# Performance work log

Measured on AMD Instinct MI355X. Metric: run time of the kernel, lower is better.

## Reference

```python
import jax, jax.numpy as jnp
import numpy as np

N_NODES = 100000
N_EDGES = 1600000
D_IN = 128
D_OUT = 128


def setup_inputs() -> dict:
    key = jax.random.key(0)
    ks = jax.random.split(key, 8)
    h = jax.random.normal(ks[0], (N_NODES, D_IN), dtype=jnp.float32)
    edge_val = jax.random.uniform(ks[1], (N_EDGES,), dtype=jnp.float32)
    # Linear weights in torch layout [out, in]
    W_self = jax.random.normal(ks[2], (D_OUT, D_IN), dtype=jnp.float32) * (1.0 / np.sqrt(D_IN))
    b_self = jax.random.normal(ks[3], (D_OUT,), dtype=jnp.float32) * 0.01
    W_nb = jax.random.normal(ks[4], (D_OUT, D_IN), dtype=jnp.float32) * (1.0 / np.sqrt(D_IN))
    b_nb = jax.random.normal(ks[5], (D_OUT,), dtype=jnp.float32) * 0.01
    edge_row = jax.random.randint(ks[6], (N_EDGES,), 0, N_NODES, dtype=jnp.int64)
    edge_col = jax.random.randint(ks[7], (N_EDGES,), 0, N_NODES, dtype=jnp.int64)
    return {"h": h, "edge_val": edge_val, "W_self": W_self, "b_self": b_self,
            "W_nb": W_nb, "b_nb": b_nb, "edge_row": edge_row, "edge_col": edge_col}


def reference(h, edge_val, W_self, b_self, W_nb, b_nb, edge_row, edge_col):
    # self_h = Linear_self(h[:out_nodes]); out_nodes == N_NODES here
    self_h = h @ W_self.T + b_self  # [N, D_OUT]
    # neighbor_h = adj.spmm(h): sparse COO (row, col, val) times dense h
    msgs = edge_val[:, None] * h[edge_col]            # [E, D_IN]
    neighbor_h = jax.ops.segment_sum(msgs, edge_row, num_segments=N_NODES)  # [N, D_IN]
    out = self_h + neighbor_h @ W_nb.T + b_nb
    return out
```

## Files before the change

kernel.cpp:

```cpp
#include <hip/hip_runtime.h>


constexpr int NN = 100000;
constexpr int NE = 1600000;
constexpr int D  = 128;
constexpr int NBUCK  = 1024;
constexpr int BROWS  = 98;
constexpr int BCAP   = 2048;
constexpr int CHUNK  = 2048;
constexpr int NCH    = (NE + CHUNK - 1) / CHUNK;
constexpr int GM     = 64;
constexpr int NT     = (NN + GM - 1) / GM;
constexpr int GRID   = 512;
constexpr int LP     = 132;

typedef __bf16 bf16x8 __attribute__((ext_vector_type(8)));
typedef float  f32x4  __attribute__((ext_vector_type(4)));
typedef float  f32x2  __attribute__((ext_vector_type(2)));
typedef unsigned short u16x4 __attribute__((ext_vector_type(4)));

__global__ __launch_bounds__(256) void gemm_mfma(
    const float* __restrict__ h,
    const float* __restrict__ Wself,
    const float* __restrict__ Wnb,
    const float* __restrict__ bself,
    const float* __restrict__ bnb,
    float* __restrict__ out,
    __bf16* __restrict__ tmpb)
{
    __shared__ __bf16 hs[2][GM * LP];
    const int t    = threadIdx.x;
    const int w    = t >> 6;
    const int lane = t & 63;
    const int l15  = lane & 15;
    const int quad = lane >> 4;

    bf16x8 wf[4][4];
    #pragma unroll
    for (int ns = 0; ns < 4; ++ns) {
        int wrow = w * 64 + ns * 16 + l15;
        const float* wr = (wrow < D) ? (Wself + (size_t)wrow * D)
                                     : (Wnb + (size_t)(wrow - D) * D);
        #pragma unroll
        for (int kk = 0; kk < 4; ++kk) {
            f32x4 lo = *(const f32x4*)(wr + kk * 32 + quad * 8);
            f32x4 hi = *(const f32x4*)(wr + kk * 32 + quad * 8 + 4);
            bf16x8 bb;
            #pragma unroll
            for (int j = 0; j < 4; ++j) { bb[j] = (__bf16)lo[j]; bb[4 + j] = (__bf16)hi[j]; }
            wf[ns][kk] = bb;
        }
    }
    f32x4 biasv[4];
    #pragma unroll
    for (int ns = 0; ns < 4; ++ns) {
        int col = w * 64 + ns * 16 + quad * 4;
        if (col < D) {
            f32x4 b1 = *(const f32x4*)(bself + col);
            f32x4 b2 = *(const f32x4*)(bnb + col);
            biasv[ns] = b1 + b2;
        } else biasv[ns] = (f32x4){0.f, 0.f, 0.f, 0.f};
    }

    int srow[4], scol[4];
    #pragma unroll
    for (int it = 0; it < 4; ++it) {
        int idx = it * 2048 + t * 8;
        srow[it] = idx >> 7;
        scol[it] = idx & 127;
    }

    {
        const int row0 = blockIdx.x * GM;
        #pragma unroll
        for (int it = 0; it < 4; ++it) {
            int gr = row0 + srow[it]; if (gr >= NN) gr = NN - 1;
            f32x4 lo = *(const f32x4*)(h + (size_t)gr * D + scol[it]);
            f32x4 hi = *(const f32x4*)(h + (size_t)gr * D + scol[it] + 4);
            bf16x8 v;
            #pragma unroll
            for (int j = 0; j < 4; ++j) { v[j] = (__bf16)lo[j]; v[4 + j] = (__bf16)hi[j]; }
            *(bf16x8*)(&hs[0][srow[it] * LP + scol[it]]) = v;
        }
    }
    __syncthreads();

    int buf = 0;
    for (int tile = blockIdx.x; tile < NT; tile += GRID) {
        const int row0 = tile * GM;
        const bool hasn = (tile + GRID) < NT;

        f32x4 pf[8];
        if (hasn) {
            const int nrow0 = (tile + GRID) * GM;
            #pragma unroll
            for (int it = 0; it < 4; ++it) {
                int gr = nrow0 + srow[it]; if (gr >= NN) gr = NN - 1;
                pf[it * 2]     = *(const f32x4*)(h + (size_t)gr * D + scol[it]);
                pf[it * 2 + 1] = *(const f32x4*)(h + (size_t)gr * D + scol[it] + 4);
            }
        }

        f32x4 acc[4][4];
        #pragma unroll
        for (int mi = 0; mi < 4; ++mi)
            #pragma unroll
            for (int ns = 0; ns < 4; ++ns) acc[mi][ns] = (f32x4){0.f, 0.f, 0.f, 0.f};

        const __bf16* hb = hs[buf];
        #pragma unroll
        for (int mi = 0; mi < 4; ++mi) {
            bf16x8 hf[4];
            #pragma unroll
            for (int kk = 0; kk < 4; ++kk)
                hf[kk] = *(const bf16x8*)(&hb[(mi * 16 + l15) * LP + quad * 8 + kk * 32]);
            #pragma unroll
            for (int ns = 0; ns < 4; ++ns)
                #pragma unroll
                for (int kk = 0; kk < 4; ++kk)
                    acc[mi][ns] = __builtin_amdgcn_mfma_f32_16x16x32_bf16(wf[ns][kk], hf[kk], acc[mi][ns], 0, 0, 0);
        }

        if (hasn) {
            #pragma unroll
            for (int it = 0; it < 4; ++it) {
                bf16x8 v;
                #pragma unroll
                for (int j = 0; j < 4; ++j) {
                    v[j]     = (__bf16)pf[it * 2][j];
                    v[4 + j] = (__bf16)pf[it * 2 + 1][j];
                }
                *(bf16x8*)(&hs[buf ^ 1][srow[it] * LP + scol[it]]) = v;
            }
        }
        __syncthreads();

        #pragma unroll
        for (int mi = 0; mi < 4; ++mi) {
            int row = row0 + mi * 16 + l15;
            if (row < NN) {
                if (w < 2) {
                    #pragma unroll
                    for (int ns = 0; ns < 4; ++ns) {
                        int col = w * 64 + ns * 16 + quad * 4;
                        *(f32x4*)(out + (size_t)row * D + col) = acc[mi][ns] + biasv[ns];
                    }
                } else {
                    #pragma unroll
                    for (int ns = 0; ns < 4; ++ns) {
                        int col = (w - 2) * 64 + ns * 16 + quad * 4;
                        u16x4 v;
                        #pragma unroll
                        for (int i = 0; i < 4; ++i) {
                            __bf16 b = (__bf16)acc[mi][ns][i];
                            v[i] = *(unsigned short*)&b;
                        }
                        *(u16x4*)(tmpb + (size_t)row * D + col) = v;
                    }
                }
            }
        }
        buf ^= 1;
    }
}

__global__ __launch_bounds__(256) void wc_scatter(
    const int* __restrict__ erow, const int* __restrict__ ecol,
    const float* __restrict__ eval_,
    int* __restrict__ gcount, int2* __restrict__ epair)
{
    __shared__ int  cnt[NBUCK];
    __shared__ int  lscan[NBUCK];
    __shared__ int  gbase[NBUCK];
    __shared__ int  ss[NBUCK];
    __shared__ int2 sbuf[CHUNK];
    __shared__ int  saddr[CHUNK];
    __shared__ int  s_total;

    const int t  = threadIdx.x;
    const int c0 = blockIdx.x * CHUNK;

    for (int b = t; b < NBUCK; b += 256) cnt[b] = 0;
    __syncthreads();

    int   bp[8];
    int   colr[8];
    float valr[8];
    #pragma unroll
    for (int j = 0; j < 8; ++j) {
        int e = c0 + j * 256 + t;
        if (e < NE) {
            int r   = erow[e];
            colr[j] = ecol[e];
            valr[j] = eval_[e];
            int b   = r / BROWS;
            int rlo = r - b * BROWS;
            int pos = atomicAdd(&cnt[b], 1);
            bp[j]   = b | (rlo << 10) | (pos << 17);
        } else bp[j] = -1;
    }
    __syncthreads();

    #pragma unroll
    for (int k = 0; k < 4; ++k) ss[t + k * 256] = cnt[t + k * 256];
    __syncthreads();
    for (int off = 1; off < NBUCK; off <<= 1) {
        int v[4];
        #pragma unroll
        for (int k = 0; k < 4; ++k) {
            int i = t + k * 256;
            v[k] = ss[i] + ((i >= off) ? ss[i - off] : 0);
        }
        __syncthreads();
        #pragma unroll
        for (int k = 0; k < 4; ++k) ss[t + k * 256] = v[k];
        __syncthreads();
    }
    #pragma unroll
    for (int k = 0; k < 4; ++k) {
        int i = t + k * 256;
        int n = cnt[i];
        lscan[i] = ss[i] - n;
        gbase[i] = (n > 0) ? atomicAdd(&gcount[i], n) : 0;
    }
    if (t == 0) s_total = ss[NBUCK - 1];
    __syncthreads();

    #pragma unroll
    for (int j = 0; j < 8; ++j) {
        if (bp[j] >= 0) {
            int b   = bp[j] & 1023;
            int rlo = (bp[j] >> 10) & 127;
            int pos = bp[j] >> 17;
            int slot = lscan[b] + pos;
            sbuf[slot]  = make_int2(colr[j] | (rlo << 17), __float_as_int(valr[j]));
            saddr[slot] = b * BCAP + gbase[b] + pos;
        }
    }
    __syncthreads();

    int ce = s_total;
    for (int i = t; i < ce; i += 256)
        epair[saddr[i]] = sbuf[i];
}

__global__ __launch_bounds__(512, 8) void sort_aggregate(
    const int2* __restrict__ epair, const int* __restrict__ gcount,
    const __bf16* __restrict__ tmpb, float* __restrict__ out)
{
    __shared__ int  cnt[BROWS];
    __shared__ int  off2[BROWS];
    __shared__ int  cur[BROWS];
    __shared__ int  ss[128];
    __shared__ int2 sorted[BCAP];

    const int t = threadIdx.x;
    const int b = blockIdx.x;
    int n = gcount[b];
    if (n > BCAP) n = BCAP;
    const int2* src = epair + (size_t)b * BCAP;

    if (t < BROWS) cnt[t] = 0;
    __syncthreads();

    int2 r[4];
    int  nr = 0;
    for (int i = t; i < n; i += 512) {
        int2 p = src[i];
        r[nr++] = p;
        atomicAdd(&cnt[(p.x >> 17) & 127], 1);
    }
    __syncthreads();

    if (t < 128) ss[t] = (t < BROWS) ? cnt[t] : 0;
    __syncthreads();
    for (int o = 1; o < 128; o <<= 1) {
        int y = 0;
        if (t < 128 && t >= o) y = ss[t - o];
        __syncthreads();
        if (t < 128) ss[t] += y;
        __syncthreads();
    }
    if (t < BROWS) {
        int v = cnt[t];
        off2[t] = ss[t] - v;
        cur[t]  = ss[t] - v;
    }
    __syncthreads();

    for (int j = 0; j < nr; ++j) {
        int slot = atomicAdd(&cur[(r[j].x >> 17) & 127], 1);
        sorted[slot] = r[j];
    }
    __syncthreads();

    const int wv   = t >> 6;
    const int lane = t & 63;
    const __bf16* tb = tmpb + lane * 2;

    for (int rl = wv; rl < BROWS; rl += 8) {
        int row = b * BROWS + rl;
        if (row >= NN) break;
        int beg = __builtin_amdgcn_readfirstlane(off2[rl]);
        int end = __builtin_amdgcn_readfirstlane(cur[rl]);
        if (beg >= end) continue;

        float ax[4] = {0.f, 0.f, 0.f, 0.f};
        float ay[4] = {0.f, 0.f, 0.f, 0.f};
        int e = beg;
        for (; e + 7 < end; e += 8) {
            int2 p[8];
            #pragma unroll
            for (int k = 0; k < 8; ++k) p[k] = sorted[e + k];
            #pragma unroll
            for (int k = 0; k < 8; ++k) {
                int col = p[k].x & 0x1FFFF;
                unsigned u = *(const unsigned*)(tb + (size_t)col * D);
                float v = __int_as_float(p[k].y);
                ax[k & 3] += v * __uint_as_float(u << 16);
                ay[k & 3] += v * __uint_as_float(u & 0xffff0000u);
            }
        }
        for (; e + 3 < end; e += 4) {
            int2 p[4];
            #pragma unroll
            for (int k = 0; k < 4; ++k) p[k] = sorted[e + k];
            #pragma unroll
            for (int k = 0; k < 4; ++k) {
                int col = p[k].x & 0x1FFFF;
                unsigned u = *(const unsigned*)(tb + (size_t)col * D);
                float v = __int_as_float(p[k].y);
                ax[k] += v * __uint_as_float(u << 16);
                ay[k] += v * __uint_as_float(u & 0xffff0000u);
            }
        }
        for (; e < end; ++e) {
            int2 p = sorted[e];
            int col = p.x & 0x1FFFF;
            unsigned u = *(const unsigned*)(tb + (size_t)col * D);
            float v = __int_as_float(p.y);
            ax[0] += v * __uint_as_float(u << 16);
            ay[0] += v * __uint_as_float(u & 0xffff0000u);
        }

        f32x2* o = (f32x2*)(out + (size_t)row * D + lane * 2);
        f32x2 c = __builtin_nontemporal_load(o);
        c.x += (ax[0] + ax[1]) + (ax[2] + ax[3]);
        c.y += (ay[0] + ay[1]) + (ay[2] + ay[3]);
        __builtin_nontemporal_store(c, o);
    }
}

extern "C" void kernel_launch(void* const* d_in, const int* in_sizes, int n_in,
                              void* d_out, int out_size, void* d_ws, size_t ws_size,
                              hipStream_t stream) {
    const float* h     = (const float*)d_in[0];
    const float* eval_ = (const float*)d_in[1];
    const float* Wself = (const float*)d_in[2];
    const float* bself = (const float*)d_in[3];
    const float* Wnb   = (const float*)d_in[4];
    const float* bnb   = (const float*)d_in[5];
    const int*   erow  = (const int*)d_in[6];
    const int*   ecol  = (const int*)d_in[7];
    float* out = (float*)d_out;

    char* p = (char*)d_ws;
    __bf16* tmpb    = (__bf16*)p;   p += (size_t)NT * GM * D * 2;
    int2*   epair   = (int2*)p;     p += (size_t)NBUCK * BCAP * 8;
    int*    gcount  = (int*)p;

    hipMemsetAsync(gcount, 0, NBUCK * 4, stream);

    gemm_mfma<<<GRID, 256, 0, stream>>>(h, Wself, Wnb, bself, bnb, out, tmpb);
    wc_scatter<<<NCH, 256, 0, stream>>>(erow, ecol, eval_, gcount, epair);
    sort_aggregate<<<NBUCK, 512, 0, stream>>>(epair, gcount, tmpb, out);
}
```

Baseline: 263.0 us.

## Merge GEMM and edge bucket-scatter into one launch; use wave-shuffle scan

Combines the MFMA GEMM kernel and the edge bucketing scatter kernel into a single launch, with the first GRID blocks doing GEMM and the rest scattering edges, sharing one union shared-memory buffer. This removes a kernel boundary and lets the compute-bound GEMM overlap the memory-bound scatter. The 1024-bucket prefix scan is also rewritten from a barrier-heavy Hillis-Steele loop over shared memory into per-thread sums plus a wavefront shuffle scan. The shared allocation is now the maximum of both roles, which can lower occupancy for the GEMM blocks.

```diff
diff --git a/kernel.cpp b/kernel.cpp
--- a/kernel.cpp
+++ b/kernel.cpp
@@ -13,235 +13,248 @@
 constexpr int NT     = (NN + GM - 1) / GM;
 constexpr int GRID   = 512;
 constexpr int LP     = 132;
+constexpr int FUSED_GRID = GRID + NCH;
 
 typedef __bf16 bf16x8 __attribute__((ext_vector_type(8)));
 typedef float  f32x4  __attribute__((ext_vector_type(4)));
 typedef float  f32x2  __attribute__((ext_vector_type(2)));
 typedef unsigned short u16x4 __attribute__((ext_vector_type(4)));
 
-__global__ __launch_bounds__(256) void gemm_mfma(
+constexpr int SMEM_BYTES = 36928;
+
+__global__ __launch_bounds__(256) void gemm_wc(
     const float* __restrict__ h,
     const float* __restrict__ Wself,
     const float* __restrict__ Wnb,
     const float* __restrict__ bself,
     const float* __restrict__ bnb,
     float* __restrict__ out,
-    __bf16* __restrict__ tmpb)
-{
-    __shared__ __bf16 hs[2][GM * LP];
-    const int t    = threadIdx.x;
-    const int w    = t >> 6;
-    const int lane = t & 63;
-    const int l15  = lane & 15;
-    const int quad = lane >> 4;
-
-    bf16x8 wf[4][4];
-    #pragma unroll
-    for (int ns = 0; ns < 4; ++ns) {
-        int wrow = w * 64 + ns * 16 + l15;
-        const float* wr = (wrow < D) ? (Wself + (size_t)wrow * D)
-                                     : (Wnb + (size_t)(wrow - D) * D);
-        #pragma unroll
-        for (int kk = 0; kk < 4; ++kk) {
-            f32x4 lo = *(const f32x4*)(wr + kk * 32 + quad * 8);
-            f32x4 hi = *(const f32x4*)(wr + kk * 32 + quad * 8 + 4);
-            bf16x8 bb;
-            #pragma unroll
-            for (int j = 0; j < 4; ++j) { bb[j] = (__bf16)lo[j]; bb[4 + j] = (__bf16)hi[j]; }
-            wf[ns][kk] = bb;
-        }
-    }
-    f32x4 biasv[4];
-    #pragma unroll
-    for (int ns = 0; ns < 4; ++ns) {
-        int col = w * 64 + ns * 16 + quad * 4;
-        if (col < D) {
-            f32x4 b1 = *(const f32x4*)(bself + col);
-            f32x4 b2 = *(const f32x4*)(bnb + col);
-            biasv[ns] = b1 + b2;
-        } else biasv[ns] = (f32x4){0.f, 0.f, 0.f, 0.f};
-    }
-
-    int srow[4], scol[4];
-    #pragma unroll
-    for (int it = 0; it < 4; ++it) {
-        int idx = it * 2048 + t * 8;
-        srow[it] = idx >> 7;
-        scol[it] = idx & 127;
-    }
-
-    {
-        const int row0 = blockIdx.x * GM;
-        #pragma unroll
-        for (int it = 0; it < 4; ++it) {
-            int gr = row0 + srow[it]; if (gr >= NN) gr = NN - 1;
-            f32x4 lo = *(const f32x4*)(h + (size_t)gr * D + scol[it]);
-            f32x4 hi = *(const f32x4*)(h + (size_t)gr * D + scol[it] + 4);
-            bf16x8 v;
-            #pragma unroll
-            for (int j = 0; j < 4; ++j) { v[j] = (__bf16)lo[j]; v[4 + j] = (__bf16)hi[j]; }
-            *(bf16x8*)(&hs[0][srow[it] * LP + scol[it]]) = v;
-        }
-    }
-    __syncthreads();
-
-    int buf = 0;
-    for (int tile = blockIdx.x; tile < NT; tile += GRID) {
-        const int row0 = tile * GM;
-        const bool hasn = (tile + GRID) < NT;
-
-        f32x4 pf[8];
-        if (hasn) {
-            const int nrow0 = (tile + GRID) * GM;
-            #pragma unroll
-            for (int it = 0; it < 4; ++it) {
-                int gr = nrow0 + srow[it]; if (gr >= NN) gr = NN - 1;
-                pf[it * 2]     = *(const f32x4*)(h + (size_t)gr * D + scol[it]);
-                pf[it * 2 + 1] = *(const f32x4*)(h + (size_t)gr * D + scol[it] + 4);
-            }
-        }
-
-        f32x4 acc[4][4];
-        #pragma unroll
-        for (int mi = 0; mi < 4; ++mi)
-            #pragma unroll
-            for (int ns = 0; ns < 4; ++ns) acc[mi][ns] = (f32x4){0.f, 0.f, 0.f, 0.f};
-
-        const __bf16* hb = hs[buf];
-        #pragma unroll
-        for (int mi = 0; mi < 4; ++mi) {
-            bf16x8 hf[4];
-            #pragma unroll
-            for (int kk = 0; kk < 4; ++kk)
-                hf[kk] = *(const bf16x8*)(&hb[(mi * 16 + l15) * LP + quad * 8 + kk * 32]);
-            #pragma unroll
-            for (int ns = 0; ns < 4; ++ns)
-                #pragma unroll
-                for (int kk = 0; kk < 4; ++kk)
-                    acc[mi][ns] = __builtin_amdgcn_mfma_f32_16x16x32_bf16(wf[ns][kk], hf[kk], acc[mi][ns], 0, 0, 0);
-        }
-
-        if (hasn) {
-            #pragma unroll
-            for (int it = 0; it < 4; ++it) {
-                bf16x8 v;
-                #pragma unroll
-                for (int j = 0; j < 4; ++j) {
-                    v[j]     = (__bf16)pf[it * 2][j];
-                    v[4 + j] = (__bf16)pf[it * 2 + 1][j];
-                }
-                *(bf16x8*)(&hs[buf ^ 1][srow[it] * LP + scol[it]]) = v;
-            }
-        }
-        __syncthreads();
-
-        #pragma unroll
-        for (int mi = 0; mi < 4; ++mi) {
-            int row = row0 + mi * 16 + l15;
-            if (row < NN) {
-                if (w < 2) {
-                    #pragma unroll
-                    for (int ns = 0; ns < 4; ++ns) {
-                        int col = w * 64 + ns * 16 + quad * 4;
-                        *(f32x4*)(out + (size_t)row * D + col) = acc[mi][ns] + biasv[ns];
-                    }
-                } else {
-                    #pragma unroll
-                    for (int ns = 0; ns < 4; ++ns) {
-                        int col = (w - 2) * 64 + ns * 16 + quad * 4;
-                        u16x4 v;
-                        #pragma unroll
-                        for (int i = 0; i < 4; ++i) {
-                            __bf16 b = (__bf16)acc[mi][ns][i];
-                            v[i] = *(unsigned short*)&b;
-                        }
-                        *(u16x4*)(tmpb + (size_t)row * D + col) = v;
-                    }
-                }
-            }
-        }
-        buf ^= 1;
-    }
-}
-
-__global__ __launch_bounds__(256) void wc_scatter(
+    __bf16* __restrict__ tmpb,
     const int* __restrict__ erow, const int* __restrict__ ecol,
     const float* __restrict__ eval_,
     int* __restrict__ gcount, int2* __restrict__ epair)
 {
-    __shared__ int  cnt[NBUCK];
-    __shared__ int  lscan[NBUCK];
-    __shared__ int  gbase[NBUCK];
-    __shared__ int  ss[NBUCK];
-    __shared__ int2 sbuf[CHUNK];
-    __shared__ int  saddr[CHUNK];
-    __shared__ int  s_total;
-
-    const int t  = threadIdx.x;
-    const int c0 = blockIdx.x * CHUNK;
-
-    for (int b = t; b < NBUCK; b += 256) cnt[b] = 0;
-    __syncthreads();
-
-    int   bp[8];
-    int   colr[8];
-    float valr[8];
-    #pragma unroll
-    for (int j = 0; j < 8; ++j) {
-        int e = c0 + j * 256 + t;
-        if (e < NE) {
-            int r   = erow[e];
-            colr[j] = ecol[e];
-            valr[j] = eval_[e];
-            int b   = r / BROWS;
-            int rlo = r - b * BROWS;
-            int pos = atomicAdd(&cnt[b], 1);
-            bp[j]   = b | (rlo << 10) | (pos << 17);
-        } else bp[j] = -1;
-    }
-    __syncthreads();
-
-    #pragma unroll
-    for (int k = 0; k < 4; ++k) ss[t + k * 256] = cnt[t + k * 256];
-    __syncthreads();
-    for (int off = 1; off < NBUCK; off <<= 1) {
-        int v[4];
+    __shared__ __align__(16) char smem[SMEM_BYTES];
+    const int t = threadIdx.x;
+
+    if (blockIdx.x < GRID) {
+        const int bid  = blockIdx.x;
+        const int w    = t >> 6;
+        const int lane = t & 63;
+        const int l15  = lane & 15;
+        const int quad = lane >> 4;
+        __bf16* hs0 = (__bf16*)smem;
+        __bf16* hs1 = hs0 + GM * LP;
+
+        bf16x8 wf[4][4];
+        #pragma unroll
+        for (int ns = 0; ns < 4; ++ns) {
+            int wrow = w * 64 + ns * 16 + l15;
+            const float* wr = (wrow < D) ? (Wself + (size_t)wrow * D)
+                                         : (Wnb + (size_t)(wrow - D) * D);
+            #pragma unroll
+            for (int kk = 0; kk < 4; ++kk) {
+                f32x4 lo = *(const f32x4*)(wr + kk * 32 + quad * 8);
+                f32x4 hi = *(const f32x4*)(wr + kk * 32 + quad * 8 + 4);
+                bf16x8 bb;
+                #pragma unroll
+                for (int j = 0; j < 4; ++j) { bb[j] = (__bf16)lo[j]; bb[4 + j] = (__bf16)hi[j]; }
+                wf[ns][kk] = bb;
+            }
+        }
+        f32x4 biasv[4];
+        #pragma unroll
+        for (int ns = 0; ns < 4; ++ns) {
+            int col = w * 64 + ns * 16 + quad * 4;
+            if (col < D) {
+                f32x4 b1 = *(const f32x4*)(bself + col);
+                f32x4 b2 = *(const f32x4*)(bnb + col);
+                biasv[ns] = b1 + b2;
+            } else biasv[ns] = (f32x4){0.f, 0.f, 0.f, 0.f};
+        }
+
+        int srow[4], scol[4];
+        #pragma unroll
+        for (int it = 0; it < 4; ++it) {
+            int idx = it * 2048 + t * 8;
+            srow[it] = idx >> 7;
+            scol[it] = idx & 127;
+        }
+
+        {
+            const int row0 = bid * GM;
+            #pragma unroll
+            for (int it = 0; it < 4; ++it) {
+                int gr = row0 + srow[it]; if (gr >= NN) gr = NN - 1;
+                f32x4 lo = *(const f32x4*)(h + (size_t)gr * D + scol[it]);
+                f32x4 hi = *(const f32x4*)(h + (size_t)gr * D + scol[it] + 4);
+                bf16x8 v;
+                #pragma unroll
+                for (int j = 0; j < 4; ++j) { v[j] = (__bf16)lo[j]; v[4 + j] = (__bf16)hi[j]; }
+                *(bf16x8*)(&hs0[srow[it] * LP + scol[it]]) = v;
+            }
+        }
+        __syncthreads();
+
+        int buf = 0;
+        for (int tile = bid; tile < NT; tile += GRID) {
+            const int row0 = tile * GM;
+            const bool hasn = (tile + GRID) < NT;
+            __bf16* hb = buf ? hs1 : hs0;
+            __bf16* hw = buf ? hs0 : hs1;
+
+            f32x4 pf[8];
+            if (hasn) {
+                const int nrow0 = (tile + GRID) * GM;
+                #pragma unroll
+                for (int it = 0; it < 4; ++it) {
+                    int gr = nrow0 + srow[it]; if (gr >= NN) gr = NN - 1;
+                    pf[it * 2]     = *(const f32x4*)(h + (size_t)gr * D + scol[it]);
+                    pf[it * 2 + 1] = *(const f32x4*)(h + (size_t)gr * D + scol[it] + 4);
+                }
+            }
+
+            f32x4 acc[4][4];
+            #pragma unroll
+            for (int mi = 0; mi < 4; ++mi)
+                #pragma unroll
+                for (int ns = 0; ns < 4; ++ns) acc[mi][ns] = (f32x4){0.f, 0.f, 0.f, 0.f};
+
+            #pragma unroll
+            for (int mi = 0; mi < 4; ++mi) {
+                bf16x8 hf[4];
+                #pragma unroll
+                for (int kk = 0; kk < 4; ++kk)
+                    hf[kk] = *(const bf16x8*)(&hb[(mi * 16 + l15) * LP + quad * 8 + kk * 32]);
+                #pragma unroll
+                for (int ns = 0; ns < 4; ++ns)
+                    #pragma unroll
+                    for (int kk = 0; kk < 4; ++kk)
+                        acc[mi][ns] = __builtin_amdgcn_mfma_f32_16x16x32_bf16(wf[ns][kk], hf[kk], acc[mi][ns], 0, 0, 0);
+            }
+
+            if (hasn) {
+                #pragma unroll
+                for (int it = 0; it < 4; ++it) {
+                    bf16x8 v;
+                    #pragma unroll
+                    for (int j = 0; j < 4; ++j) {
+                        v[j]     = (__bf16)pf[it * 2][j];
+                        v[4 + j] = (__bf16)pf[it * 2 + 1][j];
+                    }
+                    *(bf16x8*)(&hw[srow[it] * LP + scol[it]]) = v;
+                }
+            }
+            __syncthreads();
+
+            #pragma unroll
+            for (int mi = 0; mi < 4; ++mi) {
+                int row = row0 + mi * 16 + l15;
+                if (row < NN) {
+                    if (w < 2) {
+                        #pragma unroll
+                        for (int ns = 0; ns < 4; ++ns) {
+                            int col = w * 64 + ns * 16 + quad * 4;
+                            *(f32x4*)(out + (size_t)row * D + col) = acc[mi][ns] + biasv[ns];
+                        }
+                    } else {
+                        #pragma unroll
+                        for (int ns = 0; ns < 4; ++ns) {
+                            int col = (w - 2) * 64 + ns * 16 + quad * 4;
+                            u16x4 v;
+                            #pragma unroll
+                            for (int i = 0; i < 4; ++i) {
+                                __bf16 b = (__bf16)acc[mi][ns][i];
+                                v[i] = *(unsigned short*)&b;
+                            }
+                            *(u16x4*)(tmpb + (size_t)row * D + col) = v;
+                        }
+                    }
+                }
+            }
+            buf ^= 1;
+        }
+    } else {
+        int*  cnt   = (int*)smem;
+        int*  lscan = cnt + NBUCK;
+        int*  gbase = lscan + NBUCK;
+        int2* sbuf  = (int2*)(smem + 3 * NBUCK * 4);
+        int*  saddr = (int*)(smem + 3 * NBUCK * 4 + CHUNK * 8);
+        int*  wtot    = saddr + CHUNK;
+        int*  wbase_s = wtot + 4;
+        int*  s_total = wbase_s + 4;
+
+        const int wv   = t >> 6;
+        const int lane = t & 63;
+        const int c0   = (blockIdx.x - GRID) * CHUNK;
+
+        for (int b = t; b < NBUCK; b += 256) cnt[b] = 0;
+        __syncthreads();
+
+        int   bp[8];
+        int   colr[8];
+        float valr[8];
+        #pragma unroll
+        for (int j = 0; j < 8; ++j) {
+            int e = c0 + j * 256 + t;
+            if (e < NE) {
+                int r   = erow[e];
+                colr[j] = ecol[e];
+                valr[j] = eval_[e];
+                int b   = r / BROWS;
+                int rlo = r - b * BROWS;
+                int pos = atomicAdd(&cnt[b], 1);
+                bp[j]   = b | (rlo << 10) | (pos << 17);
+            } else bp[j] = -1;
+        }
+        __syncthreads();
+
+        int c4[4];
+        int pre = 0;
+        #pragma unroll
+        for (int k = 0; k < 4; ++k) { c4[k] = cnt[4 * t + k]; pre += c4[k]; }
+        int s = pre;
+        #pragma unroll
+        for (int off = 1; off < 64; off <<= 1) {
+            int y = __shfl_up(s, off, 64);
+            if (lane >= off) s += y;
+        }
+        if (lane == 63) wtot[wv] = s;
+        __syncthreads();
+        if (t == 0) {
+            int acc = 0;
+            #pragma unroll
+            for (int i = 0; i < 4; ++i) { wbase_s[i] = acc; acc += wtot[i]; }
+            *s_total = acc;
+        }
+        __syncthreads();
+        int base = wbase_s[wv] + s - pre;
         #pragma unroll
         for (int k = 0; k < 4; ++k) {
-            int i = t + k * 256;
-            v[k] = ss[i] + ((i >= off) ? ss[i - off] : 0);
-        }
-        __syncthreads();
-        #pragma unroll
-        for (int k = 0; k < 4; ++k) ss[t + k * 256] = v[k];
-        __syncthreads();
-    }
-    #pragma unroll
-    for (int k = 0; k < 4; ++k) {
-        int i = t + k * 256;
-        int n = cnt[i];
-        lscan[i] = ss[i] - n;
-        gbase[i] = (n > 0) ? atomicAdd(&gcount[i], n) : 0;
-    }
-    if (t == 0) s_total = ss[NBUCK - 1];
-    __syncthreads();
-
-    #pragma unroll
-    for (int j = 0; j < 8; ++j) {
-        if (bp[j] >= 0) {
-            int b   = bp[j] & 1023;
-            int rlo = (bp[j] >> 10) & 127;
-            int pos = bp[j] >> 17;
-            int slot = lscan[b] + pos;
-            sbuf[slot]  = make_int2(colr[j] | (rlo << 17), __float_as_int(valr[j]));
-            saddr[slot] = b * BCAP + gbase[b] + pos;
-        }
-    }
-    __syncthreads();
-
-    int ce = s_total;
-    for (int i = t; i < ce; i += 256)
-        epair[saddr[i]] = sbuf[i];
+            int i = 4 * t + k;
+            lscan[i] = base;
+            gbase[i] = (c4[k] > 0) ? atomicAdd(&gcount[i], c4[k]) : 0;
+            base += c4[k];
+        }
+        __syncthreads();
+
+        #pragma unroll
+        for (int j = 0; j < 8; ++j) {
+            if (bp[j] >= 0) {
+                int b   = bp[j] & 1023;
+                int rlo = (bp[j] >> 10) & 127;
+                int pos = bp[j] >> 17;
+                int slot = lscan[b] + pos;
+                sbuf[slot]  = make_int2(colr[j] | (rlo << 17), __float_as_int(valr[j]));
+                saddr[slot] = b * BCAP + gbase[b] + pos;
+            }
+        }
+        __syncthreads();
+
+        int ce = *s_total;
+        for (int i = t; i < ce; i += 256)
+            epair[saddr[i]] = sbuf[i];
+    }
 }
 
 __global__ __launch_bounds__(512, 8) void sort_aggregate(
@@ -371,7 +384,7 @@
 
     hipMemsetAsync(gcount, 0, NBUCK * 4, stream);
 
-    gemm_mfma<<<GRID, 256, 0, stream>>>(h, Wself, Wnb, bself, bnb, out, tmpb);
-    wc_scatter<<<NCH, 256, 0, stream>>>(erow, ecol, eval_, gcount, epair);
+    gemm_wc<<<FUSED_GRID, 256, 0, stream>>>(h, Wself, Wnb, bself, bnb, out,
+                                            tmpb, erow, ecol, eval_, gcount, epair);
     sort_aggregate<<<NBUCK, 512, 0, stream>>>(epair, gcount, tmpb, out);
 }
```

New measurement: 275.1 us. 4.6% more time.
